# Performance work log

Measured on AMD Instinct MI355X. Metric: run time of the kernel, lower is better.

The kernel has to match this reference:

```python
import jax, jax.numpy as jnp
import numpy as np

N = 50000      # nodes
E = 800000     # edges (avg degree 16)
DIN = 128
H = 128
DOUT = 64


def setup_inputs() -> dict:
    key = jax.random.key(0)
    ks = jax.random.split(key, 8)
    x = jax.random.normal(ks[0], (N, DIN), dtype=jnp.float32)
    edge_index = jax.random.randint(ks[1], (2, E), 0, N, dtype=jnp.int32)
    def glorot(k, fi, fo):
        return jax.random.normal(k, (fi, fo), dtype=jnp.float32) * (1.0 / np.sqrt(fi))
    return {
        "x": x,
        "edge_index": edge_index,
        "W1": glorot(ks[2], DIN, H), "b1": jnp.zeros((H,), jnp.float32),
        "W2": glorot(ks[3], H, H),   "b2": jnp.zeros((H,), jnp.float32),
        "W3": glorot(ks[4], H, DOUT),"b3": jnp.zeros((DOUT,), jnp.float32),
    }


def reference(x, edge_index, W1, b1, W2, b2, W3, b3):
    n = x.shape[0]
    # GCNConv: add self-loops, symmetric degree normalization D^-1/2 (A+I) D^-1/2
    loop = jnp.arange(n, dtype=edge_index.dtype)
    src = jnp.concatenate([edge_index[0], loop])  # [E+N]
    dst = jnp.concatenate([edge_index[1], loop])
    deg = jax.ops.segment_sum(jnp.ones(src.shape, x.dtype), dst, num_segments=n)
    dinv = jnp.where(deg > 0, jax.lax.rsqrt(deg), 0.0)
    norm = dinv[src] * dinv[dst]  # [E+N]

    def conv(h, W, b):
        h = h @ W                                   # [N, out]
        msg = h[src] * norm[:, None]                # gather + scale
        return jax.ops.segment_sum(msg, dst, num_segments=n) + b

    # gelu after every layer except the last (forward breaks before act)
    h = jax.nn.gelu(conv(x, W1, b1), approximate=False)
    h = jax.nn.gelu(conv(h, W2, b2), approximate=False)
    return conv(h, W3, b3)
```

## Files before the change

kernel.cpp:

```cpp
#include <hip/hip_runtime.h>
#include <math.h>

#define NDIN 128
#define NHID 128
#define NDOUT 64

typedef _Float16 half2_t __attribute__((ext_vector_type(2)));
typedef _Float16 half4_t __attribute__((ext_vector_type(4)));
typedef _Float16 half8_t __attribute__((ext_vector_type(8)));
typedef float    float4v __attribute__((ext_vector_type(4)));

__device__ __forceinline__ float gelu_exact(float x) {
    return 0.5f * x * (1.0f + erff(x * 0.70710678118654752f));
}


__device__ void wtrans_tile(const float* __restrict__ W, _Float16* __restrict__ Wt,
                            int K, int N, int bx, int by) {
    __shared__ float tile[32][33];
    int tx = threadIdx.x & 31, ty = threadIdx.x >> 5;
    for (int i = 0; i < 32; i += 8) {
        int k = by * 32 + ty + i, nn = bx * 32 + tx;
        tile[ty + i][tx] = (k < K && nn < N) ? W[(size_t)k * N + nn] : 0.f;
    }
    __syncthreads();
    for (int i = 0; i < 32; i += 8) {
        int nn = bx * 32 + ty + i, k = by * 32 + tx;
        if (nn < N && k < K) Wt[(size_t)nn * K + k] = (_Float16)tile[tx][ty + i];
    }
}

__global__ __launch_bounds__(256) void prep0_kernel(
    const float* __restrict__ W1, _Float16* __restrict__ W1t,
    const float* __restrict__ W2, _Float16* __restrict__ W2t,
    const float* __restrict__ W3, _Float16* __restrict__ W3t,
    int* __restrict__ count, int* __restrict__ done, int n) {
    int b = blockIdx.x;
    if (b < 16) {
        wtrans_tile(W1, W1t, NDIN, NHID, b & 3, b >> 2);
    } else if (b < 32) {
        wtrans_tile(W2, W2t, NHID, NHID, (b - 16) & 3, (b - 16) >> 2);
    } else if (b < 40) {
        wtrans_tile(W3, W3t, NHID, NDOUT, (b - 32) & 1, (b - 32) >> 1);
    } else {
        int z = b - 40;
        int i = z * 256 + threadIdx.x;
        if (i < n) count[i] = 0;
        if (z == 0 && threadIdx.x < 64) done[threadIdx.x] = 0;
    }
}


template <int BN>
__device__ __forceinline__ void gemm_phaseB(
    const _Float16 (*lds_a)[136], const _Float16* __restrict__ Bt,
    _Float16* __restrict__ T, int bm, int M) {
    int tid = threadIdx.x;
    int wave = tid >> 6, lane = tid & 63;
    int m = lane & 15, quad = lane >> 4;
    const int NT = BN / 16;
    float4v acc[NT];
#pragma unroll
    for (int nt = 0; nt < NT; nt++) acc[nt] = (float4v){0.f, 0.f, 0.f, 0.f};
    int arow = (wave << 4) + m;
#pragma unroll
    for (int kc = 0; kc < 128; kc += 32) {
        half8_t a = *(const half8_t*)&lds_a[arow][kc + quad * 8];
#pragma unroll
        for (int nt = 0; nt < NT; nt++) {
            half8_t b = *(const half8_t*)&Bt[(size_t)(nt * 16 + m) * 128 + kc + quad * 8];
            acc[nt] = __builtin_amdgcn_mfma_f32_16x16x32_f16(a, b, acc[nt], 0, 0, 0);
        }
    }
#pragma unroll
    for (int nt = 0; nt < NT; nt++) {
#pragma unroll
        for (int r = 0; r < 4; r++) {
            int grow = bm + (wave << 4) + (quad << 2) + r;
            if (grow < M) T[(size_t)grow * BN + nt * 16 + m] = (_Float16)acc[nt][r];
        }
    }
}


__global__ __launch_bounds__(256) void count_gemm1_kernel(
    const int* __restrict__ dst, int* __restrict__ count, int* __restrict__ eslot, int E,
    const float* __restrict__ x, const _Float16* __restrict__ W1t,
    _Float16* __restrict__ T, int M, int cblocks) {
    __shared__ _Float16 lds_a[64][136];
    int b = blockIdx.x;
    if (b < cblocks) {
        int e = b * 256 + threadIdx.x;
        if (e < E) eslot[e] = atomicAdd(&count[dst[e]], 1);
        return;
    }
    int bm = (b - cblocks) * 64;
    int tid = threadIdx.x;
#pragma unroll
    for (int j = 0; j < 8; j++) {
        int c = tid + j * 256;
        int r = c >> 5, col = (c & 31) << 2;
        int grow = bm + r;
        float4 v = make_float4(0.f, 0.f, 0.f, 0.f);
        if (grow < M) v = *(const float4*)(x + (size_t)grow * 128 + col);
        half4_t h;
        h[0] = (_Float16)v.x; h[1] = (_Float16)v.y;
        h[2] = (_Float16)v.z; h[3] = (_Float16)v.w;
        *(half4_t*)&lds_a[r][col] = h;
    }
    __syncthreads();
    gemm_phaseB<128>(lds_a, W1t, T, bm, M);
}


__global__ __launch_bounds__(256) void reduce_scan_kernel(
    const int* __restrict__ count, int* __restrict__ blocksum, int* __restrict__ blockoff,
    int* __restrict__ rowptr, float* __restrict__ dinv, int* __restrict__ done,
    int nb, int n) {
    __shared__ int s[256];
    __shared__ int flag;
    __shared__ int boff_s;
    int t = threadIdx.x;
    int i = blockIdx.x * 256 + t;
    int v = (i < n) ? count[i] : 0;
    s[t] = v;
    __syncthreads();
    for (int off = 128; off > 0; off >>= 1) {
        if (t < off) s[t] += s[t + off];
        __syncthreads();
    }
    if (t == 0) {
        atomicExch(&blocksum[blockIdx.x], s[0]);
        __threadfence();
        int old = atomicAdd(&done[0], 1);
        flag = (old == nb - 1) ? 1 : 0;
    }
    __syncthreads();
    if (flag) {
        __threadfence();
        int pv = (t < nb) ? atomicAdd(&blocksum[t], 0) : 0;
        s[t] = pv;
        __syncthreads();
        for (int off = 1; off < 256; off <<= 1) {
            int u = (t >= off) ? s[t - off] : 0;
            __syncthreads();
            s[t] += u;
            __syncthreads();
        }
        if (t < nb) atomicExch(&blockoff[t], s[t] - pv);
        if (t == 255) rowptr[n] = s[255];
        __threadfence();
        if (t == 0) atomicExch(&done[1], 1);
    } else if (t == 0) {
        while (atomicAdd(&done[1], 0) == 0) __builtin_amdgcn_s_sleep(2);
        __threadfence();
    }
    __syncthreads();
    if (t == 0) boff_s = atomicAdd(&blockoff[blockIdx.x], 0);
    s[t] = v;
    __syncthreads();
    for (int off = 1; off < 256; off <<= 1) {
        int u = (t >= off) ? s[t - off] : 0;
        __syncthreads();
        s[t] += u;
        __syncthreads();
    }
    if (i < n) {
        rowptr[i] = boff_s + s[t] - v;
        dinv[i] = rsqrtf((float)(v + 1));
    }
}


__global__ void fill_kernel(const int* __restrict__ src, const int* __restrict__ dst,
                            const int* __restrict__ eslot, const float* __restrict__ dinv,
                            const int* __restrict__ rowptr, int2* __restrict__ adj, int E) {
    int e = blockIdx.x * blockDim.x + threadIdx.x;
    if (e >= E) return;
    int s = src[e], d = dst[e];
    int p = rowptr[d] + eslot[e];
    adj[p] = make_int2(s, __float_as_int(dinv[s] * dinv[d]));
}


__device__ __forceinline__ half2_t agg_node128(
    const half2_t* __restrict__ t2, const int* __restrict__ rowptr,
    const int2* __restrict__ adj, const float* __restrict__ dinv,
    const float* __restrict__ bias, int node, int lane) {
    float wself = dinv[node];
    wself *= wself;
    half2_t v = t2[(size_t)node * 64 + lane];
    float accx = wself * (float)v[0], accy = wself * (float)v[1];
    int beg = rowptr[node], end = rowptr[node + 1];
    for (int e0 = beg; e0 < end; e0 += 64) {
        int rem = end - e0;
        int j = 0; float w = 0.f;
        if (lane < rem) {
            int2 ed = adj[e0 + lane];
            j = ed.x; w = __int_as_float(ed.y);
        }
        int cnt = rem < 64 ? rem : 64;
        for (int c = 0; c < cnt; c += 16) {
#pragma unroll
            for (int i = 0; i < 16; i++) {
                int jj = __builtin_amdgcn_readlane(j, c + i);
                float ww = __int_as_float(
                    __builtin_amdgcn_readlane(__float_as_int(w), c + i));
                half2_t u = t2[(size_t)jj * 64 + lane];
                accx += ww * (float)u[0];
                accy += ww * (float)u[1];
            }
        }
    }
    float2 b = ((const float2*)bias)[lane];
    accx = gelu_exact(accx + b.x);
    accy = gelu_exact(accy + b.y);
    half2_t o; o[0] = (_Float16)accx; o[1] = (_Float16)accy;
    return o;
}


template <int BN>
__global__ __launch_bounds__(256) void agg_gemm16_kernel(
    const _Float16* __restrict__ t, const int* __restrict__ rowptr,
    const int2* __restrict__ adj, const float* __restrict__ dinv,
    const float* __restrict__ bias, const _Float16* __restrict__ Bt,
    _Float16* __restrict__ T, int M) {
    __shared__ _Float16 lds_a[16][136];
    int tid = threadIdx.x;
    int wave = tid >> 6, lane = tid & 63;
    int bm = blockIdx.x * 16;
    const half2_t* t2 = (const half2_t*)t;
#pragma unroll 1
    for (int p = 0; p < 4; p++) {
        int r = (wave << 2) + p;
        int node = bm + r;
        half2_t o;
        o[0] = (_Float16)0.f; o[1] = (_Float16)0.f;
        if (node < M) o = agg_node128(t2, rowptr, adj, dinv, bias, node, lane);
        *(half2_t*)&lds_a[r][lane << 1] = o;
    }
    __syncthreads();

    int m = lane & 15, quad = lane >> 4;
    const int NT = BN / 64;
    float4v acc[NT];
#pragma unroll
    for (int nt = 0; nt < NT; nt++) acc[nt] = (float4v){0.f, 0.f, 0.f, 0.f};
#pragma unroll
    for (int kc = 0; kc < 128; kc += 32) {
        half8_t a = *(const half8_t*)&lds_a[m][kc + quad * 8];
#pragma unroll
        for (int nt = 0; nt < NT; nt++) {
            int col = wave * (BN / 4) + nt * 16 + m;
            half8_t b = *(const half8_t*)&Bt[(size_t)col * 128 + kc + quad * 8];
            acc[nt] = __builtin_amdgcn_mfma_f32_16x16x32_f16(a, b, acc[nt], 0, 0, 0);
        }
    }
#pragma unroll
    for (int nt = 0; nt < NT; nt++) {
#pragma unroll
        for (int r = 0; r < 4; r++) {
            int grow = bm + (quad << 2) + r;
            int col = wave * (BN / 4) + nt * 16 + m;
            if (grow < M) T[(size_t)grow * BN + col] = (_Float16)acc[nt][r];
        }
    }
}


template <int F, bool DOGELU, bool OUTF16>
__global__ __launch_bounds__(256) void agg_kernel(
    const _Float16* __restrict__ t, const int* __restrict__ rowptr,
    const int2* __restrict__ adj, const float* __restrict__ dinv,
    const float* __restrict__ bias, void* __restrict__ outp, int n) {
    int node = (int)((blockIdx.x * blockDim.x + threadIdx.x) >> 6);
    int lane = threadIdx.x & 63;
    if (node >= n) return;

    float wself = dinv[node];
    wself *= wself;
    int beg = rowptr[node];
    int end = rowptr[node + 1];

    if (F == 128) {
        const half2_t* t2 = (const half2_t*)t;
        half2_t v = t2[(size_t)node * 64 + lane];
        float accx = wself * (float)v[0], accy = wself * (float)v[1];
        for (int e0 = beg; e0 < end; e0 += 64) {
            int rem = end - e0;
            int j = 0; float w = 0.f;
            if (lane < rem) {
                int2 ed = adj[e0 + lane];
                j = ed.x; w = __int_as_float(ed.y);
            }
            int cnt = rem < 64 ? rem : 64;
            for (int c = 0; c < cnt; c += 16) {
#pragma unroll
                for (int i = 0; i < 16; i++) {
                    int jj = __builtin_amdgcn_readlane(j, c + i);
                    float ww = __int_as_float(
                        __builtin_amdgcn_readlane(__float_as_int(w), c + i));
                    half2_t u = t2[(size_t)jj * 64 + lane];
                    accx += ww * (float)u[0];
                    accy += ww * (float)u[1];
                }
            }
        }
        float2 b = ((const float2*)bias)[lane];
        accx += b.x; accy += b.y;
        if (DOGELU) { accx = gelu_exact(accx); accy = gelu_exact(accy); }
        if (OUTF16) {
            half2_t o; o[0] = (_Float16)accx; o[1] = (_Float16)accy;
            ((half2_t*)outp)[(size_t)node * 64 + lane] = o;
        } else {
            float2 o; o.x = accx; o.y = accy;
            ((float2*)outp)[(size_t)node * 64 + lane] = o;
        }
    } else {
        float acc = wself * (float)t[(size_t)node * 64 + lane];
        for (int e0 = beg; e0 < end; e0 += 64) {
            int rem = end - e0;
            int j = 0; float w = 0.f;
            if (lane < rem) {
                int2 ed = adj[e0 + lane];
                j = ed.x; w = __int_as_float(ed.y);
            }
            int cnt = rem < 64 ? rem : 64;
            for (int c = 0; c < cnt; c += 16) {
#pragma unroll
                for (int i = 0; i < 16; i++) {
                    int jj = __builtin_amdgcn_readlane(j, c + i);
                    float ww = __int_as_float(
                        __builtin_amdgcn_readlane(__float_as_int(w), c + i));
                    acc += ww * (float)t[(size_t)jj * 64 + lane];
                }
            }
        }
        acc += bias[lane];
        if (DOGELU) acc = gelu_exact(acc);
        if (OUTF16) ((_Float16*)outp)[(size_t)node * 64 + lane] = (_Float16)acc;
        else        ((float*)outp)[(size_t)node * 64 + lane] = acc;
    }
}


extern "C" void kernel_launch(void* const* d_in, const int* in_sizes, int n_in,
                              void* d_out, int out_size, void* d_ws, size_t ws_size,
                              hipStream_t stream) {
    const float* x  = (const float*)d_in[0];
    const int* edge = (const int*)d_in[1];
    const float* W1 = (const float*)d_in[2];
    const float* b1 = (const float*)d_in[3];
    const float* W2 = (const float*)d_in[4];
    const float* b2 = (const float*)d_in[5];
    const float* W3 = (const float*)d_in[6];
    const float* b3 = (const float*)d_in[7];
    float* out = (float*)d_out;

    const int N = in_sizes[0] / NDIN;
    const int E = in_sizes[1] / 2;
    const int* src = edge;
    const int* dst = edge + E;
    const int NB = (N + 255) / 256;

    char* p = (char*)d_ws;
    auto alloc = [&](size_t bytes) {
        char* q = p;
        p += (bytes + 255) & ~(size_t)255;
        return q;
    };
    int*       count    = (int*)alloc((size_t)N * 4);
    int*       rowptr   = (int*)alloc((size_t)(N + 1) * 4);
    int*       blocksum = (int*)alloc((size_t)NB * 4);
    int*       blockoff = (int*)alloc((size_t)NB * 4);
    int*       done     = (int*)alloc(256);
    float*     dinv     = (float*)alloc((size_t)N * 4);
    int*       eslot    = (int*)alloc((size_t)E * 4);
    int2*      adj      = (int2*)alloc((size_t)E * 8);
    _Float16*  W1t      = (_Float16*)alloc((size_t)NHID * NDIN * 2);
    _Float16*  W2t      = (_Float16*)alloc((size_t)NHID * NHID * 2);
    _Float16*  W3t      = (_Float16*)alloc((size_t)NDOUT * NHID * 2);
    _Float16*  tbuf     = (_Float16*)alloc((size_t)N * NHID * 2);
    _Float16*  hbuf     = (_Float16*)alloc((size_t)N * NHID * 2);

    dim3 blk(256);
    int mtiles = (N + 63) / 64;
    int ntiles16 = (N + 15) / 16;
    int eblocks = (E + 255) / 256;
    int agg_blocks = (N + 3) / 4;

    prep0_kernel<<<40 + NB, blk, 0, stream>>>(W1, W1t, W2, W2t, W3, W3t, count, done, N);
    count_gemm1_kernel<<<eblocks + mtiles, blk, 0, stream>>>(
        dst, count, eslot, E, x, W1t, tbuf, N, eblocks);
    reduce_scan_kernel<<<NB, blk, 0, stream>>>(count, blocksum, blockoff, rowptr,
                                               dinv, done, NB, N);
    fill_kernel<<<eblocks, blk, 0, stream>>>(src, dst, eslot, dinv, rowptr, adj, E);
    agg_gemm16_kernel<128><<<ntiles16, blk, 0, stream>>>(tbuf, rowptr, adj, dinv, b1,
                                                         W2t, hbuf, N);
    agg_gemm16_kernel<64><<<ntiles16, blk, 0, stream>>>(hbuf, rowptr, adj, dinv, b2,
                                                        W3t, tbuf, N);
    agg_kernel<64, false, false><<<agg_blocks, blk, 0, stream>>>(tbuf, rowptr, adj,
                                                                 dinv, b3, out, N);
}
```

Before: 269.7 us.

## Build CSR via two-level bucket sort instead of global atomic counting

```diff
diff --git a/kernel.cpp b/kernel.cpp
--- a/kernel.cpp
+++ b/kernel.cpp
@@ -34,7 +34,7 @@
     const float* __restrict__ W1, _Float16* __restrict__ W1t,
     const float* __restrict__ W2, _Float16* __restrict__ W2t,
     const float* __restrict__ W3, _Float16* __restrict__ W3t,
-    int* __restrict__ count, int* __restrict__ done, int n) {
+    int* __restrict__ done) {
     int b = blockIdx.x;
     if (b < 16) {
         wtrans_tile(W1, W1t, NDIN, NHID, b & 3, b >> 2);
@@ -43,10 +43,7 @@
     } else if (b < 40) {
         wtrans_tile(W3, W3t, NHID, NDOUT, (b - 32) & 1, (b - 32) >> 1);
     } else {
-        int z = b - 40;
-        int i = z * 256 + threadIdx.x;
-        if (i < n) count[i] = 0;
-        if (z == 0 && threadIdx.x < 64) done[threadIdx.x] = 0;
+        if (threadIdx.x < 64) done[threadIdx.x] = 0;
     }
 }
 
@@ -83,19 +80,24 @@
 }
 
 
-__global__ __launch_bounds__(256) void count_gemm1_kernel(
-    const int* __restrict__ dst, int* __restrict__ count, int* __restrict__ eslot, int E,
+__global__ __launch_bounds__(256) void hist_gemm1_kernel(
+    const int* __restrict__ dst, int* __restrict__ hist, int E,
     const float* __restrict__ x, const _Float16* __restrict__ W1t,
-    _Float16* __restrict__ T, int M, int cblocks) {
+    _Float16* __restrict__ T, int M, int hblocks) {
     __shared__ _Float16 lds_a[64][136];
+    __shared__ int h[256];
     int b = blockIdx.x;
-    if (b < cblocks) {
-        int e = b * 256 + threadIdx.x;
-        if (e < E) eslot[e] = atomicAdd(&count[dst[e]], 1);
+    int tid = threadIdx.x;
+    if (b < hblocks) {
+        h[tid] = 0;
+        __syncthreads();
+        int e = b * 256 + tid;
+        if (e < E) atomicAdd(&h[dst[e] >> 8], 1);
+        __syncthreads();
+        hist[b * 256 + tid] = h[tid];
         return;
     }
-    int bm = (b - cblocks) * 64;
-    int tid = threadIdx.x;
+    int bm = (b - hblocks) * 64;
 #pragma unroll
     for (int j = 0; j < 8; j++) {
         int c = tid + j * 256;
@@ -103,83 +105,131 @@
         int grow = bm + r;
         float4 v = make_float4(0.f, 0.f, 0.f, 0.f);
         if (grow < M) v = *(const float4*)(x + (size_t)grow * 128 + col);
-        half4_t h;
-        h[0] = (_Float16)v.x; h[1] = (_Float16)v.y;
-        h[2] = (_Float16)v.z; h[3] = (_Float16)v.w;
-        *(half4_t*)&lds_a[r][col] = h;
+        half4_t hh;
+        hh[0] = (_Float16)v.x; hh[1] = (_Float16)v.y;
+        hh[2] = (_Float16)v.z; hh[3] = (_Float16)v.w;
+        *(half4_t*)&lds_a[r][col] = hh;
     }
     __syncthreads();
     gemm_phaseB<128>(lds_a, W1t, T, bm, M);
 }
 
 
-__global__ __launch_bounds__(256) void reduce_scan_kernel(
-    const int* __restrict__ count, int* __restrict__ blocksum, int* __restrict__ blockoff,
-    int* __restrict__ rowptr, float* __restrict__ dinv, int* __restrict__ done,
-    int nb, int n) {
-    __shared__ int s[256];
-    __shared__ int flag;
-    __shared__ int boff_s;
-    int t = threadIdx.x;
-    int i = blockIdx.x * 256 + t;
-    int v = (i < n) ? count[i] : 0;
-    s[t] = v;
-    __syncthreads();
-    for (int off = 128; off > 0; off >>= 1) {
-        if (t < off) s[t] += s[t + off];
-        __syncthreads();
-    }
-    if (t == 0) {
-        atomicExch(&blocksum[blockIdx.x], s[0]);
-        __threadfence();
-        int old = atomicAdd(&done[0], 1);
-        flag = (old == nb - 1) ? 1 : 0;
-    }
-    __syncthreads();
-    if (flag) {
-        __threadfence();
-        int pv = (t < nb) ? atomicAdd(&blocksum[t], 0) : 0;
-        s[t] = pv;
-        __syncthreads();
-        for (int off = 1; off < 256; off <<= 1) {
+__global__ __launch_bounds__(1024) void bscan_kernel(
+    int* __restrict__ hist, int* __restrict__ btotal, int* __restrict__ bbase,
+    int* __restrict__ done, int EB, int nbk) {
+    __shared__ int s[1024];
+    __shared__ int carry;
+    int b = blockIdx.x, t = threadIdx.x;
+    if (t == 0) carry = 0;
+    __syncthreads();
+    for (int c0 = 0; c0 < EB; c0 += 1024) {
+        int blk = c0 + t;
+        int v = (blk < EB) ? hist[blk * 256 + b] : 0;
+        s[t] = v;
+        __syncthreads();
+        for (int off = 1; off < 1024; off <<= 1) {
             int u = (t >= off) ? s[t - off] : 0;
             __syncthreads();
             s[t] += u;
             __syncthreads();
         }
-        if (t < nb) atomicExch(&blockoff[t], s[t] - pv);
-        if (t == 255) rowptr[n] = s[255];
+        if (blk < EB) hist[blk * 256 + b] = carry + (s[t] - v);
+        int ctot = s[1023];
+        __syncthreads();
+        if (t == 0) carry += ctot;
+        __syncthreads();
+    }
+    if (t == 0) {
+        atomicExch(&btotal[b], carry);
         __threadfence();
-        if (t == 0) atomicExch(&done[1], 1);
-    } else if (t == 0) {
-        while (atomicAdd(&done[1], 0) == 0) __builtin_amdgcn_s_sleep(2);
-        __threadfence();
-    }
-    __syncthreads();
-    if (t == 0) boff_s = atomicAdd(&blockoff[blockIdx.x], 0);
-    s[t] = v;
+        int old = atomicAdd(&done[0], 1);
+        if (old == nbk - 1) {
+            int acc = 0;
+            for (int i = 0; i < nbk; i++) {
+                int ti = atomicAdd(&btotal[i], 0);
+                bbase[i] = acc;
+                acc += ti;
+            }
+            bbase[nbk] = acc;
+        }
+    }
+}
+
+
+__global__ __launch_bounds__(256) void scatter_kernel(
+    const int* __restrict__ src, const int* __restrict__ dst,
+    const int* __restrict__ hist, const int* __restrict__ bbase,
+    int2* __restrict__ tmp, int E) {
+    __shared__ int rank[256];
+    int t = threadIdx.x;
+    rank[t] = 0;
+    __syncthreads();
+    int blk = blockIdx.x;
+    int e = blk * 256 + t;
+    if (e < E) {
+        int d = dst[e];
+        int b = d >> 8;
+        int lr = atomicAdd(&rank[b], 1);
+        int pos = bbase[b] + hist[blk * 256 + b] + lr;
+        tmp[pos] = make_int2(src[e], d);
+    }
+}
+
+
+__global__ __launch_bounds__(1024) void bcsr_a_kernel(
+    const int2* __restrict__ tmp, const int* __restrict__ bbase,
+    int* __restrict__ rowptr, float* __restrict__ dinv, int N, int E) {
+    __shared__ int cnt[256];
+    __shared__ int loc[256];
+    int b = blockIdx.x, t = threadIdx.x;
+    if (t < 256) cnt[t] = 0;
+    __syncthreads();
+    int base = bbase[b], end = bbase[b + 1];
+    for (int i = base + t; i < end; i += 1024)
+        atomicAdd(&cnt[tmp[i].y & 255], 1);
+    __syncthreads();
+    if (t < 256) loc[t] = cnt[t];
     __syncthreads();
     for (int off = 1; off < 256; off <<= 1) {
-        int u = (t >= off) ? s[t - off] : 0;
-        __syncthreads();
-        s[t] += u;
-        __syncthreads();
-    }
-    if (i < n) {
-        rowptr[i] = boff_s + s[t] - v;
-        dinv[i] = rsqrtf((float)(v + 1));
-    }
-}
-
-
-__global__ void fill_kernel(const int* __restrict__ src, const int* __restrict__ dst,
-                            const int* __restrict__ eslot, const float* __restrict__ dinv,
-                            const int* __restrict__ rowptr, int2* __restrict__ adj, int E) {
-    int e = blockIdx.x * blockDim.x + threadIdx.x;
-    if (e >= E) return;
-    int s = src[e], d = dst[e];
-    int p = rowptr[d] + eslot[e];
-    adj[p] = make_int2(s, __float_as_int(dinv[s] * dinv[d]));
+        int u = (t < 256 && t >= off) ? loc[t - off] : 0;
+        __syncthreads();
+        if (t < 256) loc[t] += u;
+        __syncthreads();
+    }
+    int d0 = b * 256;
+    if (t < 256 && d0 + t < N) {
+        rowptr[d0 + t] = base + loc[t] - cnt[t];
+        dinv[d0 + t] = rsqrtf((float)(cnt[t] + 1));
+    }
+    if (b == 0 && t == 0) rowptr[N] = E;
+}
+
+
+__global__ __launch_bounds__(1024) void bcsr_b_kernel(
+    const int2* __restrict__ tmp, const int* __restrict__ bbase,
+    const int* __restrict__ rowptr, const float* __restrict__ dinv,
+    int2* __restrict__ adj, int N) {
+    __shared__ int rank[256];
+    __shared__ float dloc[256];
+    __shared__ int rploc[256];
+    int b = blockIdx.x, t = threadIdx.x;
+    int d0 = b * 256;
+    if (t < 256) {
+        rank[t] = 0;
+        bool v = (d0 + t < N);
+        dloc[t] = v ? dinv[d0 + t] : 0.f;
+        rploc[t] = v ? rowptr[d0 + t] : 0;
+    }
+    __syncthreads();
+    int base = bbase[b], end = bbase[b + 1];
+    for (int i = base + t; i < end; i += 1024) {
+        int2 ed = tmp[i];
+        int j = ed.y & 255;
+        float w = dinv[ed.x] * dloc[j];
+        int r = atomicAdd(&rank[j], 1);
+        adj[rploc[j] + r] = make_int2(ed.x, __float_as_int(w));
+    }
 }
 
 
@@ -362,7 +412,8 @@
     const int E = in_sizes[1] / 2;
     const int* src = edge;
     const int* dst = edge + E;
-    const int NB = (N + 255) / 256;
+    const int NBK = (N + 255) >> 8;
+    const int EB  = (E + 255) / 256;
 
     char* p = (char*)d_ws;
     auto alloc = [&](size_t bytes) {
@@ -370,13 +421,13 @@
         p += (bytes + 255) & ~(size_t)255;
         return q;
     };
-    int*       count    = (int*)alloc((size_t)N * 4);
+    int*       hist     = (int*)alloc((size_t)EB * 256 * 4);
+    int*       btotal   = (int*)alloc((size_t)NBK * 4);
+    int*       bbase    = (int*)alloc((size_t)(NBK + 1) * 4);
+    int*       done     = (int*)alloc(256);
     int*       rowptr   = (int*)alloc((size_t)(N + 1) * 4);
-    int*       blocksum = (int*)alloc((size_t)NB * 4);
-    int*       blockoff = (int*)alloc((size_t)NB * 4);
-    int*       done     = (int*)alloc(256);
     float*     dinv     = (float*)alloc((size_t)N * 4);
-    int*       eslot    = (int*)alloc((size_t)E * 4);
+    int2*      tmp      = (int2*)alloc((size_t)E * 8);
     int2*      adj      = (int2*)alloc((size_t)E * 8);
     _Float16*  W1t      = (_Float16*)alloc((size_t)NHID * NDIN * 2);
     _Float16*  W2t      = (_Float16*)alloc((size_t)NHID * NHID * 2);
@@ -385,17 +436,18 @@
     _Float16*  hbuf     = (_Float16*)alloc((size_t)N * NHID * 2);
 
     dim3 blk(256);
+    dim3 blk1k(1024);
     int mtiles = (N + 63) / 64;
     int ntiles16 = (N + 15) / 16;
-    int eblocks = (E + 255) / 256;
     int agg_blocks = (N + 3) / 4;
 
-    prep0_kernel<<<40 + NB, blk, 0, stream>>>(W1, W1t, W2, W2t, W3, W3t, count, done, N);
-    count_gemm1_kernel<<<eblocks + mtiles, blk, 0, stream>>>(
-        dst, count, eslot, E, x, W1t, tbuf, N, eblocks);
-    reduce_scan_kernel<<<NB, blk, 0, stream>>>(count, blocksum, blockoff, rowptr,
-                                               dinv, done, NB, N);
-    fill_kernel<<<eblocks, blk, 0, stream>>>(src, dst, eslot, dinv, rowptr, adj, E);
+    prep0_kernel<<<41, blk, 0, stream>>>(W1, W1t, W2, W2t, W3, W3t, done);
+    hist_gemm1_kernel<<<EB + mtiles, blk, 0, stream>>>(dst, hist, E, x, W1t,
+                                                       tbuf, N, EB);
+    bscan_kernel<<<NBK, blk1k, 0, stream>>>(hist, btotal, bbase, done, EB, NBK);
+    scatter_kernel<<<EB, blk, 0, stream>>>(src, dst, hist, bbase, tmp, E);
+    bcsr_a_kernel<<<NBK, blk1k, 0, stream>>>(tmp, bbase, rowptr, dinv, N, E);
+    bcsr_b_kernel<<<NBK, blk1k, 0, stream>>>(tmp, bbase, rowptr, dinv, adj, N);
     agg_gemm16_kernel<128><<<ntiles16, blk, 0, stream>>>(tbuf, rowptr, adj, dinv, b1,
                                                          W2t, hbuf, N);
     agg_gemm16_kernel<64><<<ntiles16, blk, 0, stream>>>(hbuf, rowptr, adj, dinv, b2,
```

New measurement: 282.4 us. +4.7%, slower.
